# Kernel tuning notes

Measured on AMD Instinct MI355X. Metric: run time of the kernel, lower is better.

Reference implementation:

```python
import jax, jax.numpy as jnp
from jax import lax
import numpy as np

B, T, F_IN, H = 64, 128, 12, 128  # batch, seq_len, input/output features, hidden


def _uinit(key, shape, fan):
    return jax.random.uniform(key, shape, jnp.float32, -1.0, 1.0) / np.float32(np.sqrt(fan))


def setup_inputs() -> dict:
    key = jax.random.key(0)
    ks = jax.random.split(key, 12)
    inp = {
        "x": jax.random.normal(ks[0], (B, T, F_IN), jnp.float32),
        # encoder LSTM (gate order i,f,g,o; b = b_ih + b_hh folded together)
        "enc_Wih": _uinit(ks[1], (4 * H, F_IN), H),
        "enc_Whh": _uinit(ks[2], (4 * H, H), H),
        "enc_b": _uinit(ks[3], (4 * H,), H),
        # decoder LSTM (input is the 12-dim teacher-forced x slice)
        "dec_Wih": _uinit(ks[4], (4 * H, F_IN), H),
        "dec_Whh": _uinit(ks[5], (4 * H, H), H),
        "dec_b": _uinit(ks[6], (4 * H,), H),
        # attention: Linear(2H -> H) with bias, then v: Linear(H -> 1, no bias)
        "attn_W": _uinit(ks[7], (H, 2 * H), 2 * H),
        "attn_b": _uinit(ks[8], (H,), 2 * H),
        "v_w": _uinit(ks[9], (H,), H),
        # output layer: Linear(2H -> F_IN)  (intended width; see notes)
        "out_W": _uinit(ks[10], (F_IN, 2 * H), 2 * H),
        "out_b": _uinit(ks[11], (F_IN,), 2 * H),
    }
    return inp


def _lstm_cell(xt, h, c, Wih, Whh, b):
    z = xt @ Wih.T + h @ Whh.T + b  # [B, 4H]
    i, f, g, o = jnp.split(z, 4, axis=-1)
    c = jax.nn.sigmoid(f) * c + jax.nn.sigmoid(i) * jnp.tanh(g)
    h = jax.nn.sigmoid(o) * jnp.tanh(c)
    return h, c


def reference(x, enc_Wih, enc_Whh, enc_b, dec_Wih, dec_Whh, dec_b,
              attn_W, attn_b, v_w, out_W, out_b):
    b_, t_, _ = x.shape
    hdim = enc_Whh.shape[1]
    xs = jnp.swapaxes(x, 0, 1)  # [T, B, F]
    h0 = jnp.zeros((b_, hdim), x.dtype)
    c0 = jnp.zeros((b_, hdim), x.dtype)

    def enc_step(carry, xt):
        h, c = carry
        h, c = _lstm_cell(xt, h, c, enc_Wih, enc_Whh, enc_b)
        return (h, c), h

    (hT, cT), enc_hs = lax.scan(enc_step, (h0, c0), xs)
    enc_out = jnp.swapaxes(enc_hs, 0, 1)  # [B, T, H]

    # split attn weight: cat(hidden, enc_out) @ W.T == hidden@W1.T + enc_out@W2.T
    W1, W2 = attn_W[:, :hdim], attn_W[:, hdim:]
    enc_proj = jnp.einsum("bth,gh->btg", enc_out, W2)  # precompute encoder side

    def dec_step(carry, xt):
        h, c = carry
        h, c = _lstm_cell(xt, h, c, dec_Wih, dec_Whh, dec_b)
        energy = jnp.tanh((h @ W1.T)[:, None, :] + enc_proj + attn_b)  # [B,T,H]
        score = jnp.einsum("bth,h->bt", energy, v_w)
        w = jax.nn.softmax(score, axis=1)  # attention over encoder time
        ctx = jnp.einsum("bt,bth->bh", w, enc_out)
        return (h, c), jnp.concatenate([h, ctx], axis=-1)  # [B, 2H]

    _, dec_ys = lax.scan(dec_step, (hT, cT), xs)
    dec_out = jnp.swapaxes(dec_ys, 0, 1)  # [B, T, 2H]
    return dec_out @ out_W.T + out_b  # [B, T, F]
```

## Files before the change

kernel.cpp:

```cpp
#include <hip/hip_runtime.h>
#include <hip/hip_bf16.h>

#define BB 64
#define TT 128
#define FIN 12
#define HH 128

#define LOG2E 1.4426950408889634f
#define TWO_LOG2E 2.8853900817779268f

__device__ __forceinline__ float fexp2(float x) { return __builtin_amdgcn_exp2f(x); }
__device__ __forceinline__ float frcp(float x)  { return __builtin_amdgcn_rcpf(x); }

__device__ __forceinline__ float tanh_f(float x) {
  return 1.0f - 2.0f * frcp(1.0f + fexp2(TWO_LOG2E * x));
}
__device__ __forceinline__ float sigm_f(float x) {
  return frcp(1.0f + fexp2(-LOG2E * x));
}

template <int CTRL>
__device__ __forceinline__ float dpp_addstage(float v) {
  int s = __builtin_amdgcn_update_dpp(0, __float_as_int(v), CTRL, 0xF, 0xF, true);
  return v + __int_as_float(s);
}
__device__ __forceinline__ float red8(float v) {
  v = dpp_addstage<0xB1>(v);
  v = dpp_addstage<0x4E>(v);
  v = dpp_addstage<0x141>(v);
  return v;
}

#define FMA4S(acc, s, v) do { \
  acc.x = fmaf((s), (v).x, acc.x); \
  acc.y = fmaf((s), (v).y, acc.y); \
  acc.z = fmaf((s), (v).z, acc.z); \
  acc.w = fmaf((s), (v).w, acc.w); } while (0)

#define ACC4(hv, wv, a) do { \
  a = fmaf((hv).x, (wv).x, a); a = fmaf((hv).y, (wv).y, a); \
  a = fmaf((hv).z, (wv).z, a); a = fmaf((hv).w, (wv).w, a); } while (0)

__device__ __forceinline__ void lstm_phase(
    const float* __restrict__ Wih, const float* __restrict__ Whh,
    const float* __restrict__ bias, float* __restrict__ Hout ,
    float* __restrict__ xs, float (*hbuf)[160], float* __restrict__ hist,
    const int tid, const int q, const int i, float& c)
{
  const int xo   = (q < 4) ? 3 * q : 0;
  const float xz = (q < 4) ? 1.0f : 0.0f;

  float4 wg[4][4];
  #pragma unroll
  for (int g = 0; g < 4; ++g)
    #pragma unroll
    for (int j = 0; j < 4; ++j)
      wg[g][j] = *(const float4*)(Whh + ((g * HH + i) * HH) + 16 * q + 4 * j);

  float wx[4][3];
  #pragma unroll
  for (int g = 0; g < 4; ++g)
    #pragma unroll
    for (int j = 0; j < 3; ++j)
      wx[g][j] = Wih[(g * HH + i) * FIN + xo + j] * xz;

  const float bi = bias[i], bf = bias[HH + i], bg = bias[2 * HH + i], bo = bias[3 * HH + i];

  int ts = 0;
  #pragma unroll 1
  for (int half = 0; half < 2; ++half) {
    #pragma unroll 1
    for (int tt = 0; tt < 64; ++tt, ++ts) {
      const int t = half * 64 + tt;
      __syncthreads();
      const float* hb = (const float*)hbuf[ts & 1] + q * 20;
      float4 h0 = *(const float4*)(hb + 0);
      float4 h1 = *(const float4*)(hb + 4);
      float4 h2 = *(const float4*)(hb + 8);
      float4 h3 = *(const float4*)(hb + 12);

      const float* xt = xs + t * FIN + xo;
      float x0 = xt[0], x1 = xt[1], x2 = xt[2];
      float ai = wx[0][0] * x0 + wx[0][1] * x1 + wx[0][2] * x2;
      float af = wx[1][0] * x0 + wx[1][1] * x1 + wx[1][2] * x2;
      float ag = wx[2][0] * x0 + wx[2][1] * x1 + wx[2][2] * x2;
      float ao = wx[3][0] * x0 + wx[3][1] * x1 + wx[3][2] * x2;

      ACC4(h0, wg[0][0], ai); ACC4(h0, wg[1][0], af); ACC4(h0, wg[2][0], ag); ACC4(h0, wg[3][0], ao);
      ACC4(h1, wg[0][1], ai); ACC4(h1, wg[1][1], af); ACC4(h1, wg[2][1], ag); ACC4(h1, wg[3][1], ao);
      ACC4(h2, wg[0][2], ai); ACC4(h2, wg[1][2], af); ACC4(h2, wg[2][2], ag); ACC4(h2, wg[3][2], ao);
      ACC4(h3, wg[0][3], ai); ACC4(h3, wg[1][3], af); ACC4(h3, wg[2][3], ag); ACC4(h3, wg[3][3], ao);

      ai = red8(ai); af = red8(af); ag = red8(ag); ao = red8(ao);

      if (q == 0) {
        float zi = sigm_f(ai + bi);
        float zf = sigm_f(af + bf);
        float zg = tanh_f(ag + bg);
        float zo = sigm_f(ao + bo);
        c = fmaf(zf, c, zi * zg);
        float hn = zo * tanh_f(c);
        hbuf[(ts + 1) & 1][(i >> 4) * 20 + (i & 15)] = hn;
        hist[tt * HH + i] = hn;
      }
    }
    __syncthreads();
    {
      float4* dst = (float4*)(Hout + (size_t)(half * 64) * HH);
      const float4* src = (const float4*)hist;
      dst[tid]        = src[tid];
      dst[tid + 1024] = src[tid + 1024];
    }
  }
}

__global__ __launch_bounds__(1024, 4) void lstm_enc_kernel(
    const float* __restrict__ x,
    const float* __restrict__ eWih, const float* __restrict__ eWhh, const float* __restrict__ eb,
    float* __restrict__ encH, float* __restrict__ decH)
{
  const int b   = blockIdx.x;
  const int tid = threadIdx.x;
  const int q   = tid & 7;
  const int i   = tid >> 3;

  __shared__ __align__(16) float xs[TT * FIN];
  __shared__ __align__(16) float hbuf[2][160];
  __shared__ __align__(16) float hist[64 * HH];

  if (tid < (TT * FIN / 4))
    ((float4*)xs)[tid] = ((const float4*)(x + (size_t)b * TT * FIN))[tid];
  if (tid < 320) ((float*)hbuf)[tid] = 0.0f;
  float c = 0.0f;

  lstm_phase(eWih, eWhh, eb, encH + (size_t)b * TT * HH, xs, hbuf, hist, tid, q, i, c);

  if (q == 0) decH[(size_t)b * TT * HH + i] = c;
}

__global__ __launch_bounds__(1024, 4) void lstm_dec_p_kernel(
    const float* __restrict__ x,
    const float* __restrict__ dWih, const float* __restrict__ dWhh, const float* __restrict__ db,
    const float* __restrict__ attnW,
    const float* __restrict__ encH,
    float* __restrict__ decH, float* __restrict__ Pbuf)
{
  __shared__ __align__(16) float smem[12416];
  const int tid = threadIdx.x;

  if (blockIdx.x < 64) {
    const int b = blockIdx.x;
    const int q = tid & 7;
    const int i = tid >> 3;
    float* xs           = smem;
    float (*hbuf)[160]  = (float(*)[160])(smem + 1536);
    float* hist         = smem + 1856;

    if (tid < (TT * FIN / 4))
      ((float4*)xs)[tid] = ((const float4*)(x + (size_t)b * TT * FIN))[tid];
    if (tid < 128) {
      float hv = encH[((size_t)b * TT + 127) * HH + tid];
      hbuf[0][(tid >> 4) * 20 + (tid & 15)] = hv;
    }
    float c = 0.0f;
    if (q == 0) c = decH[(size_t)b * TT * HH + i];

    lstm_phase(dWih, dWhh, db, decH + (size_t)b * TT * HH, xs, hbuf, hist, tid, q, i, c);
  } else {
    const int pb = blockIdx.x - 64;
    const int b  = pb & 63;
    const int r0 = (pb >> 6) * 64;
    float* WT = smem;
    float* Xt = smem + 4224;

    const float* X = encH + ((size_t)b * TT + r0) * HH;
    ((float4*)Xt)[tid]        = ((const float4*)X)[tid];
    ((float4*)Xt)[tid + 1024] = ((const float4*)X)[tid + 1024];

    const float* W = attnW + HH;
    const int hq = tid & 31, rr = tid >> 5;
    const int h0 = 4 * hq;

    float4 acc0 = make_float4(0.f, 0.f, 0.f, 0.f);
    float4 acc1 = acc0;

    #pragma unroll 1
    for (int kb = 0; kb < 4; ++kb) {
      __syncthreads();
      {
        int h = tid >> 3, koff = (tid & 7) * 4;
        float4 v = *(const float4*)(W + h * 256 + kb * 32 + koff);
        WT[(koff + 0) * 132 + h] = v.x;
        WT[(koff + 1) * 132 + h] = v.y;
        WT[(koff + 2) * 132 + h] = v.z;
        WT[(koff + 3) * 132 + h] = v.w;
      }
      __syncthreads();
      const float* xr0 = Xt + (2 * rr) * 128 + kb * 32;
      const float* xr1 = xr0 + 128;
      #pragma unroll
      for (int k4 = 0; k4 < 32; k4 += 4) {
        float4 xa = *(const float4*)(xr0 + k4);
        float4 xb = *(const float4*)(xr1 + k4);
        float4 w0 = *(const float4*)&WT[(k4 + 0) * 132 + h0];
        float4 w1 = *(const float4*)&WT[(k4 + 1) * 132 + h0];
        float4 w2 = *(const float4*)&WT[(k4 + 2) * 132 + h0];
        float4 w3 = *(const float4*)&WT[(k4 + 3) * 132 + h0];
        FMA4S(acc0, xa.x, w0); FMA4S(acc0, xa.y, w1);
        FMA4S(acc0, xa.z, w2); FMA4S(acc0, xa.w, w3);
        FMA4S(acc1, xb.x, w0); FMA4S(acc1, xb.y, w1);
        FMA4S(acc1, xb.z, w2); FMA4S(acc1, xb.w, w3);
      }
    }
    acc0.x = fexp2(TWO_LOG2E * acc0.x); acc0.y = fexp2(TWO_LOG2E * acc0.y);
    acc0.z = fexp2(TWO_LOG2E * acc0.z); acc0.w = fexp2(TWO_LOG2E * acc0.w);
    acc1.x = fexp2(TWO_LOG2E * acc1.x); acc1.y = fexp2(TWO_LOG2E * acc1.y);
    acc1.z = fexp2(TWO_LOG2E * acc1.z); acc1.w = fexp2(TWO_LOG2E * acc1.w);
    float* O = Pbuf + ((size_t)b * TT + r0) * HH;
    *(float4*)(O + (2 * rr) * 128 + h0)     = acc0;
    *(float4*)(O + (2 * rr + 1) * 128 + h0) = acc1;
  }
}

__global__ __launch_bounds__(256, 2) void projA_kernel(
    const float* __restrict__ decH, const float* __restrict__ attnW,
    const float* __restrict__ attnb, float* __restrict__ Abuf)
{
  const int b  = blockIdx.x & 63;
  const int r0 = (blockIdx.x >> 6) * 16;
  const int tid = threadIdx.x;

  __shared__ __align__(16) float WT[64 * 128];
  __shared__ __align__(16) float Xt[16 * 128];

  const float* X = decH + ((size_t)b * TT + r0) * HH;
  const float* W = attnW;

  ((float4*)Xt)[tid]       = ((const float4*)X)[tid];
  ((float4*)Xt)[256 + tid] = ((const float4*)X)[256 + tid];

  const int hq = tid & 31, rr = tid >> 5;
  const int h0 = 4 * hq;

  float4 acc0 = *(const float4*)(attnb + h0);
  float4 acc1 = acc0;

  for (int kb = 0; kb < 2; ++kb) {
    __syncthreads();
    {
      int h = tid >> 1, koff = (tid & 1) * 32;
      #pragma unroll
      for (int j = 0; j < 8; ++j) {
        float4 v = *(const float4*)(W + h * 256 + kb * 64 + koff + 4 * j);
        int kp = koff + 4 * j;
        WT[(kp + 0) * 128 + h] = v.x;
        WT[(kp + 1) * 128 + h] = v.y;
        WT[(kp + 2) * 128 + h] = v.z;
        WT[(kp + 3) * 128 + h] = v.w;
      }
    }
    __syncthreads();
    const float* xr0 = Xt + (2 * rr) * 128 + kb * 64;
    const float* xr1 = xr0 + 128;
    #pragma unroll
    for (int k4 = 0; k4 < 64; k4 += 4) {
      float4 xa = *(const float4*)(xr0 + k4);
      float4 xb = *(const float4*)(xr1 + k4);
      float4 w0 = *(const float4*)&WT[(k4 + 0) * 128 + h0];
      float4 w1 = *(const float4*)&WT[(k4 + 1) * 128 + h0];
      float4 w2 = *(const float4*)&WT[(k4 + 2) * 128 + h0];
      float4 w3 = *(const float4*)&WT[(k4 + 3) * 128 + h0];
      FMA4S(acc0, xa.x, w0); FMA4S(acc0, xa.y, w1);
      FMA4S(acc0, xa.z, w2); FMA4S(acc0, xa.w, w3);
      FMA4S(acc1, xb.x, w0); FMA4S(acc1, xb.y, w1);
      FMA4S(acc1, xb.z, w2); FMA4S(acc1, xb.w, w3);
    }
  }
  acc0.x = fexp2(TWO_LOG2E * acc0.x); acc0.y = fexp2(TWO_LOG2E * acc0.y);
  acc0.z = fexp2(TWO_LOG2E * acc0.z); acc0.w = fexp2(TWO_LOG2E * acc0.w);
  acc1.x = fexp2(TWO_LOG2E * acc1.x); acc1.y = fexp2(TWO_LOG2E * acc1.y);
  acc1.z = fexp2(TWO_LOG2E * acc1.z); acc1.w = fexp2(TWO_LOG2E * acc1.w);
  float* O = Abuf + ((size_t)b * TT + r0) * HH;
  *(float4*)(O + (2 * rr) * 128 + h0)     = acc0;
  *(float4*)(O + (2 * rr + 1) * 128 + h0) = acc1;
}

#define AST 132
#define Y2ST 20

__global__ __launch_bounds__(512, 2) void attn_kernel(
    const float* __restrict__ encH, const float* __restrict__ decH,
    const float* __restrict__ Pbuf, const float* __restrict__ Abuf,
    const float* __restrict__ vw, const float* __restrict__ outW,
    const float* __restrict__ outb, float* __restrict__ out)
{
  const int b  = blockIdx.x >> 3;
  const int s0 = (blockIdx.x & 7) * 16;
  const int tid = threadIdx.x;

  __shared__ __align__(16) float buf[64 * 128];
  __shared__ __align__(16) float a_lds[16 * AST];
  __shared__ __align__(16) float sc[16 * AST];
  __shared__ __align__(16) float dh[16 * 128];
  __shared__ __align__(16) float vl[HH];
  __shared__ __align__(16) float y2s[TT * Y2ST];
  __shared__ __align__(16) float w2l[12 * AST];

  ((float4*)dh)[tid] = ((const float4*)(decH + ((size_t)b * TT + s0) * HH))[tid];
  if (tid < 32) ((float4*)vl)[tid] = ((const float4*)vw)[tid];
  {
    int r = tid >> 5, c4 = (tid & 31) * 4;
    float4 av = *(const float4*)(Abuf + ((size_t)b * TT + s0 + r) * HH + c4);
    *(float4*)&a_lds[r * AST + c4] = av;
  }
  if (tid < 384) {
    int f = tid >> 5, k = (tid & 31) * 4;
    float4 wv = *(const float4*)(outW + f * 256 + 128 + k);
    *(float4*)&w2l[f * AST + k] = wv;
  }

  const int u  = tid & 31;
  const int sl = tid >> 5;
  const int uq = u & 15;
  const int uh = u >> 4;

  for (int half = 0; half < 2; ++half) {
    const int tbase = half * 64;
    __syncthreads();
    #pragma unroll
    for (int i = 0; i < 4; ++i) {
      int flat = i * 2048 + tid * 4;
      int tp = flat >> 7;
      int h0 = flat & 127;
      float4 v = *(const float4*)(Pbuf + ((size_t)b * TT + tbase + tp) * HH + h0);
      int tq = tp >> 2, tr = tp & 3;
      buf[(h0 + 0) * 64 + 4 * ((tq ^ ((h0 + 0) >> 2)) & 15) + tr] = v.x;
      buf[(h0 + 1) * 64 + 4 * ((tq ^ ((h0 + 1) >> 2)) & 15) + tr] = v.y;
      buf[(h0 + 2) * 64 + 4 * ((tq ^ ((h0 + 2) >> 2)) & 15) + tr] = v.z;
      buf[(h0 + 3) * 64 + 4 * ((tq ^ ((h0 + 3) >> 2)) & 15) + tr] = v.w;
    }
    __syncthreads();
    float4 acc = make_float4(0.f, 0.f, 0.f, 0.f);
    const float* earow = a_lds + sl * AST;
    #pragma unroll 4
    for (int hh = 0; hh < 64; hh += 4) {
      const int h = uh * 64 + hh;
      float4 ea = *(const float4*)&earow[h];
      float4 va = *(const float4*)&vl[h];
      const int xoff = 4 * ((uq ^ ((h >> 2) & 15)) & 15);
      float4 p0 = *(const float4*)&buf[(h + 0) * 64 + xoff];
      float4 p1 = *(const float4*)&buf[(h + 1) * 64 + xoff];
      float4 p2 = *(const float4*)&buf[(h + 2) * 64 + xoff];
      float4 p3 = *(const float4*)&buf[(h + 3) * 64 + xoff];
      acc.x = fmaf(va.x, frcp(fmaf(ea.x, p0.x, 1.f)), acc.x);
      acc.y = fmaf(va.x, frcp(fmaf(ea.x, p0.y, 1.f)), acc.y);
      acc.z = fmaf(va.x, frcp(fmaf(ea.x, p0.z, 1.f)), acc.z);
      acc.w = fmaf(va.x, frcp(fmaf(ea.x, p0.w, 1.f)), acc.w);
      acc.x = fmaf(va.y, frcp(fmaf(ea.y, p1.x, 1.f)), acc.x);
      acc.y = fmaf(va.y, frcp(fmaf(ea.y, p1.y, 1.f)), acc.y);
      acc.z = fmaf(va.y, frcp(fmaf(ea.y, p1.z, 1.f)), acc.z);
      acc.w = fmaf(va.y, frcp(fmaf(ea.y, p1.w, 1.f)), acc.w);
      acc.x = fmaf(va.z, frcp(fmaf(ea.z, p2.x, 1.f)), acc.x);
      acc.y = fmaf(va.z, frcp(fmaf(ea.z, p2.y, 1.f)), acc.y);
      acc.z = fmaf(va.z, frcp(fmaf(ea.z, p2.z, 1.f)), acc.z);
      acc.w = fmaf(va.z, frcp(fmaf(ea.z, p2.w, 1.f)), acc.w);
      acc.x = fmaf(va.w, frcp(fmaf(ea.w, p3.x, 1.f)), acc.x);
      acc.y = fmaf(va.w, frcp(fmaf(ea.w, p3.y, 1.f)), acc.y);
      acc.z = fmaf(va.w, frcp(fmaf(ea.w, p3.z, 1.f)), acc.z);
      acc.w = fmaf(va.w, frcp(fmaf(ea.w, p3.w, 1.f)), acc.w);
    }
    acc.x += __shfl_xor(acc.x, 16, 64);
    acc.y += __shfl_xor(acc.y, 16, 64);
    acc.z += __shfl_xor(acc.z, 16, 64);
    acc.w += __shfl_xor(acc.w, 16, 64);
    if (uh == 0) {
      float4 o;
      o.x = -2.f * acc.x; o.y = -2.f * acc.y;
      o.z = -2.f * acc.z; o.w = -2.f * acc.w;
      *(float4*)&sc[sl * AST + tbase + 4 * uq] = o;
    }
  }
  __syncthreads();

  {
    float4 sv = *(const float4*)&sc[sl * AST + 4 * u];
    float mx = fmaxf(fmaxf(sv.x, sv.y), fmaxf(sv.z, sv.w));
    #pragma unroll
    for (int msk = 1; msk <= 16; msk <<= 1) mx = fmaxf(mx, __shfl_xor(mx, msk, 64));
    float4 e;
    e.x = fexp2(LOG2E * (sv.x - mx));
    e.y = fexp2(LOG2E * (sv.y - mx));
    e.z = fexp2(LOG2E * (sv.z - mx));
    e.w = fexp2(LOG2E * (sv.w - mx));
    float sm = (e.x + e.y) + (e.z + e.w);
    #pragma unroll
    for (int msk = 1; msk <= 16; msk <<= 1) sm += __shfl_xor(sm, msk, 64);
    float r = frcp(sm);
    e.x *= r; e.y *= r; e.z *= r; e.w *= r;
    *(float4*)&sc[sl * AST + 4 * u] = e;
  }

  for (int half = 0; half < 2; ++half) {
    const int tbase = half * 64;
    __syncthreads();
    #pragma unroll
    for (int i = 0; i < 4; ++i) {
      int flat = i * 2048 + tid * 4;
      int tp = flat >> 7;
      int hh0 = flat & 127;
      *(float4*)&buf[tp * 128 + hh0] =
          *(const float4*)(encH + ((size_t)b * TT + tbase + tp) * HH + hh0);
    }
    __syncthreads();
    {
      int j = tid;
      int t = j / 12, f = j - 12 * t;
      float a = 0.f;
      const float* br = buf + t * 128;
      const float* wr = w2l + f * AST;
      #pragma unroll 8
      for (int k = 0; k < 32; ++k) {
        float4 bv = *(const float4*)(br + 4 * k);
        float4 wv = *(const float4*)(wr + 4 * k);
        ACC4(bv, wv, a);
      }
      y2s[(tbase + t) * Y2ST + f] = a;
      if (tid < 256) {
        int j2 = tid + 512;
        int t2 = j2 / 12, f2 = j2 - 12 * t2;
        float a2 = 0.f;
        const float* br2 = buf + t2 * 128;
        const float* wr2 = w2l + f2 * AST;
        #pragma unroll 8
        for (int k = 0; k < 32; ++k) {
          float4 bv = *(const float4*)(br2 + 4 * k);
          float4 wv = *(const float4*)(wr2 + 4 * k);
          ACC4(bv, wv, a2);
        }
        y2s[(tbase + t2) * Y2ST + f2] = a2;
      }
    }
  }
  __syncthreads();

  if (tid < 192) {
    int s = tid / 12, f = tid - 12 * (tid / 12);
    float acc = outb[f];
    const float4* w4 = (const float4*)(outW + f * 256);
    const float4* d4 = (const float4*)(dh + s * 128);
    #pragma unroll
    for (int k = 0; k < 32; ++k) {
      float4 wv = w4[k], dv = d4[k];
      acc = fmaf(wv.x, dv.x, acc); acc = fmaf(wv.y, dv.y, acc);
      acc = fmaf(wv.z, dv.z, acc); acc = fmaf(wv.w, dv.w, acc);
    }
    const float* wrow = sc + s * AST;
    #pragma unroll 8
    for (int t = 0; t < TT; ++t)
      acc = fmaf(wrow[t], y2s[t * Y2ST + f], acc);
    out[((size_t)b * TT + s0 + s) * FIN + f] = acc;
  }
}

extern "C" void kernel_launch(void* const* d_in, const int* in_sizes, int n_in,
                              void* d_out, int out_size, void* d_ws, size_t ws_size,
                              hipStream_t stream)
{
  const float* x     = (const float*)d_in[0];
  const float* eWih  = (const float*)d_in[1];
  const float* eWhh  = (const float*)d_in[2];
  const float* eb    = (const float*)d_in[3];
  const float* dWih  = (const float*)d_in[4];
  const float* dWhh  = (const float*)d_in[5];
  const float* db    = (const float*)d_in[6];
  const float* attnW = (const float*)d_in[7];
  const float* attnb = (const float*)d_in[8];
  const float* vw    = (const float*)d_in[9];
  const float* outW  = (const float*)d_in[10];
  const float* outb  = (const float*)d_in[11];
  float* out = (float*)d_out;

  float* ws   = (float*)d_ws;
  const size_t SEG = (size_t)BB * TT * HH;
  float* encH = ws;
  float* decH = ws + SEG;
  float* Pbuf = ws + 2 * SEG;
  float* Abuf = ws + 3 * SEG;

  lstm_enc_kernel<<<64, 1024, 0, stream>>>(x, eWih, eWhh, eb, encH, decH);
  lstm_dec_p_kernel<<<192, 1024, 0, stream>>>(x, dWih, dWhh, db, attnW, encH, decH, Pbuf);
  projA_kernel<<<512, 256, 0, stream>>>(decH, attnW, attnb, Abuf);
  attn_kernel<<<512, 512, 0, stream>>>(encH, decH, Pbuf, Abuf, vw, outW, outb, out);
}
```

Baseline: 326.4 us.

## Precompute encoder output-projection once in spare decoder-kernel blocks

The context-side output projection (enc_out times the second half of out_W) was recomputed by each of the 8 attention blocks per batch. It is now computed once per batch by 64 extra blocks in the decoder LSTM kernel, which run alongside the latency-bound recurrence, and stored in a new workspace buffer. The attention kernel then loads the precomputed values instead of staging encH and doing the dot products. The new path needs a larger workspace and falls back to the old path when the workspace is too small.

```diff
diff --git a/kernel.cpp b/kernel.cpp
--- a/kernel.cpp
+++ b/kernel.cpp
@@ -141,9 +141,9 @@
 __global__ __launch_bounds__(1024, 4) void lstm_dec_p_kernel(
     const float* __restrict__ x,
     const float* __restrict__ dWih, const float* __restrict__ dWhh, const float* __restrict__ db,
-    const float* __restrict__ attnW,
+    const float* __restrict__ attnW, const float* __restrict__ outW,
     const float* __restrict__ encH,
-    float* __restrict__ decH, float* __restrict__ Pbuf)
+    float* __restrict__ decH, float* __restrict__ Pbuf, float* __restrict__ y2buf)
 {
   __shared__ __align__(16) float smem[12416];
   const int tid = threadIdx.x;
@@ -166,7 +166,7 @@
     if (q == 0) c = decH[(size_t)b * TT * HH + i];
 
     lstm_phase(dWih, dWhh, db, decH + (size_t)b * TT * HH, xs, hbuf, hist, tid, q, i, c);
-  } else {
+  } else if (blockIdx.x < 192) {
     const int pb = blockIdx.x - 64;
     const int b  = pb & 63;
     const int r0 = (pb >> 6) * 64;
@@ -219,6 +219,28 @@
     float* O = Pbuf + ((size_t)b * TT + r0) * HH;
     *(float4*)(O + (2 * rr) * 128 + h0)     = acc0;
     *(float4*)(O + (2 * rr + 1) * 128 + h0) = acc1;
+  } else if (y2buf) {
+    const int b = blockIdx.x - 192;
+    float* w2l = smem;
+    if (tid < 384) {
+      int f = tid >> 5, k = (tid & 31) * 4;
+      float4 wv = *(const float4*)(outW + f * 256 + 128 + k);
+      *(float4*)&w2l[f * 132 + k] = wv;
+    }
+    __syncthreads();
+    for (int j = tid; j < TT * 12; j += 1024) {
+      int t = j / 12, f = j - 12 * t;
+      const float* er = encH + ((size_t)b * TT + t) * HH;
+      const float* wr = w2l + f * 132;
+      float a = 0.f;
+      #pragma unroll 8
+      for (int k = 0; k < 32; ++k) {
+        float4 ev = *(const float4*)(er + 4 * k);
+        float4 wv = *(const float4*)(wr + 4 * k);
+        ACC4(ev, wv, a);
+      }
+      y2buf[b * (TT * 16) + t * 16 + f] = a;
+    }
   }
 }
 
@@ -288,9 +310,11 @@
 #define AST 132
 #define Y2ST 20
 
+template <bool HY2>
 __global__ __launch_bounds__(512, 2) void attn_kernel(
     const float* __restrict__ encH, const float* __restrict__ decH,
     const float* __restrict__ Pbuf, const float* __restrict__ Abuf,
+    const float* __restrict__ y2buf,
     const float* __restrict__ vw, const float* __restrict__ outW,
     const float* __restrict__ outb, float* __restrict__ out)
 {
@@ -313,10 +337,18 @@
     float4 av = *(const float4*)(Abuf + ((size_t)b * TT + s0 + r) * HH + c4);
     *(float4*)&a_lds[r * AST + c4] = av;
   }
-  if (tid < 384) {
-    int f = tid >> 5, k = (tid & 31) * 4;
-    float4 wv = *(const float4*)(outW + f * 256 + 128 + k);
-    *(float4*)&w2l[f * AST + k] = wv;
+  if constexpr (HY2) {
+    if (tid < 512) {
+      float4 v = ((const float4*)(y2buf + (size_t)b * (TT * 16)))[tid];
+      int t = tid >> 2, g = (tid & 3) * 4;
+      *(float4*)&y2s[t * Y2ST + g] = v;
+    }
+  } else {
+    if (tid < 384) {
+      int f = tid >> 5, k = (tid & 31) * 4;
+      float4 wv = *(const float4*)(outW + f * 256 + 128 + k);
+      *(float4*)&w2l[f * AST + k] = wv;
+    }
   }
 
   const int u  = tid & 31;
@@ -400,44 +432,46 @@
     *(float4*)&sc[sl * AST + 4 * u] = e;
   }
 
-  for (int half = 0; half < 2; ++half) {
-    const int tbase = half * 64;
-    __syncthreads();
-    #pragma unroll
-    for (int i = 0; i < 4; ++i) {
-      int flat = i * 2048 + tid * 4;
-      int tp = flat >> 7;
-      int hh0 = flat & 127;
-      *(float4*)&buf[tp * 128 + hh0] =
-          *(const float4*)(encH + ((size_t)b * TT + tbase + tp) * HH + hh0);
-    }
-    __syncthreads();
-    {
-      int j = tid;
-      int t = j / 12, f = j - 12 * t;
-      float a = 0.f;
-      const float* br = buf + t * 128;
-      const float* wr = w2l + f * AST;
-      #pragma unroll 8
-      for (int k = 0; k < 32; ++k) {
-        float4 bv = *(const float4*)(br + 4 * k);
-        float4 wv = *(const float4*)(wr + 4 * k);
-        ACC4(bv, wv, a);
-      }
-      y2s[(tbase + t) * Y2ST + f] = a;
-      if (tid < 256) {
-        int j2 = tid + 512;
-        int t2 = j2 / 12, f2 = j2 - 12 * t2;
-        float a2 = 0.f;
-        const float* br2 = buf + t2 * 128;
-        const float* wr2 = w2l + f2 * AST;
+  if constexpr (!HY2) {
+    for (int half = 0; half < 2; ++half) {
+      const int tbase = half * 64;
+      __syncthreads();
+      #pragma unroll
+      for (int i = 0; i < 4; ++i) {
+        int flat = i * 2048 + tid * 4;
+        int tp = flat >> 7;
+        int hh0 = flat & 127;
+        *(float4*)&buf[tp * 128 + hh0] =
+            *(const float4*)(encH + ((size_t)b * TT + tbase + tp) * HH + hh0);
+      }
+      __syncthreads();
+      {
+        int j = tid;
+        int t = j / 12, f = j - 12 * t;
+        float a = 0.f;
+        const float* br = buf + t * 128;
+        const float* wr = w2l + f * AST;
         #pragma unroll 8
         for (int k = 0; k < 32; ++k) {
-          float4 bv = *(const float4*)(br2 + 4 * k);
-          float4 wv = *(const float4*)(wr2 + 4 * k);
-          ACC4(bv, wv, a2);
+          float4 bv = *(const float4*)(br + 4 * k);
+          float4 wv = *(const float4*)(wr + 4 * k);
+          ACC4(bv, wv, a);
         }
-        y2s[(tbase + t2) * Y2ST + f2] = a2;
+        y2s[(tbase + t) * Y2ST + f] = a;
+        if (tid < 256) {
+          int j2 = tid + 512;
+          int t2 = j2 / 12, f2 = j2 - 12 * t2;
+          float a2 = 0.f;
+          const float* br2 = buf + t2 * 128;
+          const float* wr2 = w2l + f2 * AST;
+          #pragma unroll 8
+          for (int k = 0; k < 32; ++k) {
+            float4 bv = *(const float4*)(br2 + 4 * k);
+            float4 wv = *(const float4*)(wr2 + 4 * k);
+            ACC4(bv, wv, a2);
+          }
+          y2s[(tbase + t2) * Y2ST + f2] = a2;
+        }
       }
     }
   }
@@ -486,9 +520,23 @@
   float* decH = ws + SEG;
   float* Pbuf = ws + 2 * SEG;
   float* Abuf = ws + 3 * SEG;
+  float* y2buf = ws + 4 * SEG;
+
+  const size_t need_bytes = (4 * SEG + (size_t)BB * TT * 16) * sizeof(float);
+  const bool have_y2 = ws_size >= need_bytes;
 
   lstm_enc_kernel<<<64, 1024, 0, stream>>>(x, eWih, eWhh, eb, encH, decH);
-  lstm_dec_p_kernel<<<192, 1024, 0, stream>>>(x, dWih, dWhh, db, attnW, encH, decH, Pbuf);
-  projA_kernel<<<512, 256, 0, stream>>>(decH, attnW, attnb, Abuf);
-  attn_kernel<<<512, 512, 0, stream>>>(encH, decH, Pbuf, Abuf, vw, outW, outb, out);
-}
+  if (have_y2) {
+    lstm_dec_p_kernel<<<256, 1024, 0, stream>>>(x, dWih, dWhh, db, attnW, outW,
+                                                encH, decH, Pbuf, y2buf);
+    projA_kernel<<<512, 256, 0, stream>>>(decH, attnW, attnb, Abuf);
+    attn_kernel<true><<<512, 512, 0, stream>>>(encH, decH, Pbuf, Abuf, y2buf,
+                                               vw, outW, outb, out);
+  } else {
+    lstm_dec_p_kernel<<<192, 1024, 0, stream>>>(x, dWih, dWhh, db, attnW, outW,
+                                                encH, decH, Pbuf, nullptr);
+    projA_kernel<<<512, 256, 0, stream>>>(decH, attnW, attnb, Abuf);
+    attn_kernel<false><<<512, 512, 0, stream>>>(encH, decH, Pbuf, Abuf, nullptr,
+                                                vw, outW, outb, out);
+  }
+}
```

New measurement: 314.9 us (median of 2 runs). -3.5%, faster.
